# Kernel tuning notes

Hardware: AMD Instinct MI355X
Metric: run time of the kernel (lower is better)

Reference implementation:

```python
import jax, jax.numpy as jnp
import numpy as np

N_NODES = 100000
N_EDGES = 1600000
IN_DIM = 256
HID_DIM = 64
NUM_CLASSES = 32
NEG_SLOPE = 0.01  # F.leaky_relu default


def setup_inputs() -> dict:
    key = jax.random.key(0)
    k1, k2, k3, k4, k5, k6 = jax.random.split(key, 6)
    return {
        "local_features": jax.random.normal(k1, (N_NODES, IN_DIM), dtype=jnp.float32),
        "edge_index": jax.random.randint(k2, (2, N_EDGES), 0, N_NODES, dtype=jnp.int64),
        "weight1": jax.random.uniform(k3, (IN_DIM, HID_DIM), dtype=jnp.float32),
        "weight2": jax.random.uniform(k4, (HID_DIM, NUM_CLASSES), dtype=jnp.float32),
        "att_weight1": jax.random.uniform(k5, (2 * HID_DIM, 1), dtype=jnp.float32),
        "att_weight2": jax.random.uniform(k6, (2 * NUM_CLASSES, 1), dtype=jnp.float32),
    }


def _gat_attention_aggregate(H, a, src, dst, n_nodes):
    # H: [N, D], a: [2D, 1]. Edge score = leaky_relu([H_src||H_dst] @ a)
    # computed without materializing [E, 2D]: split a into src/dst halves.
    d = H.shape[1]
    s_score = (H @ a[:d]).squeeze(-1)   # [N]
    d_score = (H @ a[d:]).squeeze(-1)   # [N]
    e = jax.nn.leaky_relu(s_score[src] + d_score[dst], NEG_SLOPE)  # [E]
    # segment softmax over each row (grouped by src), as torch.sparse.softmax(dim=1)
    m = jax.ops.segment_max(e, src, num_segments=n_nodes)          # [N]
    ex = jnp.exp(e - m[src])                                       # [E]
    denom = jax.ops.segment_sum(ex, src, num_segments=n_nodes)     # [N]
    att = ex / denom[src]                                          # [E]
    # sparse mm: out[i] = sum_{(i,j) in E} att_ij * H[j]
    return jax.ops.segment_sum(att[:, None] * H[dst], src, num_segments=n_nodes)


def reference(local_features, edge_index, weight1, weight2, att_weight1, att_weight2):
    src, dst = edge_index[0], edge_index[1]
    n = local_features.shape[0]
    Hw1 = local_features @ weight1                                  # [N, HID]
    hidden = jax.nn.elu(_gat_attention_aggregate(Hw1, att_weight1, src, dst, n))
    Hw2 = hidden @ weight2                                          # [N, C]
    out = _gat_attention_aggregate(Hw2, att_weight2, src, dst, n)
    return jax.nn.log_softmax(out, axis=1)
```

## Files before the change

kernel.cpp:

```cpp
#include <hip/hip_runtime.h>
#include <math.h>

#define IN_DIM 256
#define HID 64
#define NC 32
#define NEG 0.01f
#define INF_NEG -1e30f
#define SX 36
#define SX2 68
#define MAXNBK 512
#define SLOT 8256
#define BCAP 12288
#define BIN_CHUNK 4096

static inline int ceil_div(int a, int b){ return (a + b - 1) / b; }

static __device__ __forceinline__ float lrelu(float x){ return x > 0.f ? x : NEG * x; }


__global__ __launch_bounds__(256) void bin_kernel(const int* __restrict__ src,
      const int* __restrict__ dst, int* __restrict__ cursor,
      unsigned int* __restrict__ tmp, int E, int nbk){
  __shared__ unsigned int payload[BIN_CHUNK];
  __shared__ unsigned short bid[BIN_CHUNK];
  __shared__ int cnt[MAXNBK];
  __shared__ int lofs[MAXNBK];
  __shared__ int gbase[MAXNBK];
  __shared__ int s2[256];
  int tid = threadIdx.x;
  int beg = blockIdx.x * BIN_CHUNK;
  int end = min(E, beg + BIN_CHUNK);
  int len = end - beg;

  for (int i = tid; i < MAXNBK; i += 256) cnt[i] = 0;
  __syncthreads();
  for (int e = beg + tid; e < end; e += 256)
    atomicAdd(&cnt[src[e] >> 8], 1);
  __syncthreads();
  int a0 = cnt[2 * tid], a1 = cnt[2 * tid + 1];
  int pair = a0 + a1;
  s2[tid] = pair; __syncthreads();
  int val = pair;
  for (int off = 1; off < 256; off <<= 1){
    int add = (tid >= off) ? s2[tid - off] : 0;
    __syncthreads();
    val += add; s2[tid] = val;
    __syncthreads();
  }
  int ep = val - pair;
  lofs[2 * tid] = ep;
  lofs[2 * tid + 1] = ep + a0;
  __syncthreads();
  for (int i = tid; i < nbk; i += 256){
    int c = cnt[i];
    gbase[i] = (c > 0) ? atomicAdd(&cursor[i], c) : 0;
  }
  __syncthreads();
  for (int i = tid; i < MAXNBK; i += 256) cnt[i] = 0;
  __syncthreads();
  for (int e = beg + tid; e < end; e += 256){
    int s = src[e];
    int b = s >> 8;
    int r = atomicAdd(&cnt[b], 1);
    int pos = lofs[b] + r;
    payload[pos] = ((unsigned)(s & 255) << 17) | (unsigned)dst[e];
    bid[pos] = (unsigned short)b;
  }
  __syncthreads();
  for (int pos = tid; pos < len; pos += 256){
    int b = bid[pos];
    int idx = pos - lofs[b];
    int g = gbase[b] + idx;
    if (g < SLOT) tmp[(size_t)b * SLOT + g] = payload[pos];
  }
}

__global__ __launch_bounds__(512) void bucket_base_kernel(const int* __restrict__ cursor,
      int* __restrict__ bbase, int nbk){
  __shared__ int sh[512];
  int tid = threadIdx.x;
  int v = (tid < nbk) ? min(cursor[tid], SLOT) : 0;
  sh[tid] = v; __syncthreads();
  int val = v;
  for (int off = 1; off < 512; off <<= 1){
    int add = (tid >= off) ? sh[tid - off] : 0;
    __syncthreads();
    val += add; sh[tid] = val;
    __syncthreads();
  }
  if (tid < nbk) bbase[tid] = val - v;
}

__global__ __launch_bounds__(256) void bucket_scatter_kernel(const unsigned int* __restrict__ tmp,
      const int* __restrict__ cursor, const int* __restrict__ bbase,
      int* __restrict__ row_ptr, int* __restrict__ csr, int n){
  __shared__ int cnt[256];
  __shared__ int cur[256];
  __shared__ int lbuf[BCAP];
  int tid = threadIdx.x;
  int b = blockIdx.x;
  int n0 = b << 8;
  int nn = min(256, n - n0);
  int len = min(cursor[b], SLOT);
  int segb = bbase[b];
  const unsigned int* T = tmp + (size_t)b * SLOT;
  cnt[tid] = 0;
  __syncthreads();
  for (int e = tid; e < len; e += 256) atomicAdd(&cnt[T[e] >> 17], 1);
  __syncthreads();
  int tv = cnt[tid];
  int val = tv;
  for (int off = 1; off < 256; off <<= 1){
    int add = (tid >= off) ? cnt[tid - off] : 0;
    __syncthreads();
    val += add; cnt[tid] = val;
    __syncthreads();
  }
  int excl = val - tv;
  cur[tid] = excl;
  if (tid < nn) row_ptr[n0 + tid] = segb + excl;
  if (n0 + nn == n && tid == 0) row_ptr[n] = segb + len;
  __syncthreads();
  if (len <= BCAP){
    for (int e = tid; e < len; e += 256){
      unsigned v = T[e];
      int pos = atomicAdd(&cur[v >> 17], 1);
      lbuf[pos] = (int)(v & 0x1FFFF);
    }
    __syncthreads();
    for (int e = tid; e < len; e += 256) csr[segb + e] = lbuf[e];
  } else {
    for (int e = tid; e < len; e += 256){
      unsigned v = T[e];
      int pos = atomicAdd(&cur[v >> 17], 1);
      csr[segb + pos] = (int)(v & 0x1FFFF);
    }
  }
}


__global__ void hist_kernel(const int* __restrict__ src, int* __restrict__ counts, int E){
  int i = blockIdx.x * blockDim.x + threadIdx.x;
  if (i < E) atomicAdd(&counts[src[i]], 1);
}
__global__ void scan_blocks_kernel(const int* __restrict__ counts, int* __restrict__ excl,
                                   int* __restrict__ bsums, int n){
  __shared__ int sh[256];
  int tid = threadIdx.x;
  int base = blockIdx.x * 1024 + tid * 4;
  int c[4]; int tsum = 0;
  #pragma unroll
  for (int j = 0; j < 4; j++){ int i = base + j; c[j] = (i < n) ? counts[i] : 0; tsum += c[j]; }
  sh[tid] = tsum; __syncthreads();
  int val = tsum;
  for (int off = 1; off < 256; off <<= 1){
    int add = (tid >= off) ? sh[tid - off] : 0;
    __syncthreads();
    val += add; sh[tid] = val;
    __syncthreads();
  }
  int p = val - tsum;
  #pragma unroll
  for (int j = 0; j < 4; j++){ int i = base + j; if (i < n) excl[i] = p; p += c[j]; }
  if (tid == 255) bsums[blockIdx.x] = val;
}
__global__ void scan_sums_kernel(int* __restrict__ bsums, int* __restrict__ row_ptr,
                                 int nb, int n, int E){
  __shared__ int sh[256];
  int tid = threadIdx.x;
  int v = (tid < nb) ? bsums[tid] : 0;
  sh[tid] = v; __syncthreads();
  int val = v;
  for (int off = 1; off < 256; off <<= 1){
    int add = (tid >= off) ? sh[tid - off] : 0;
    __syncthreads();
    val += add; sh[tid] = val;
    __syncthreads();
  }
  if (tid < nb) bsums[tid] = val - v;
  if (tid == 0) row_ptr[n] = E;
}
__global__ void add_offsets_kernel(int* __restrict__ excl, const int* __restrict__ bsums, int n){
  int i = blockIdx.x * 1024 + threadIdx.x;
  if (i < n) excl[i] += bsums[blockIdx.x];
}
__global__ void scatter_kernel(const int* __restrict__ src, const int* __restrict__ dst,
                               const int* __restrict__ row_ptr, int* __restrict__ fill,
                               int* __restrict__ csr, int E){
  int i = blockIdx.x * blockDim.x + threadIdx.x;
  if (i >= E) return;
  int s = src[i];
  int pos = row_ptr[s] + atomicAdd(&fill[s], 1);
  csr[pos] = dst[i];
}


__global__ __launch_bounds__(256) void gemm1_kernel(const float* __restrict__ X, const float* __restrict__ W,
      const float* __restrict__ a, float* __restrict__ H,
      float* __restrict__ svec, float* __restrict__ dvec, int n){
  __shared__ float xs[64 * SX];
  __shared__ float ws[32 * 64];
  int tid = threadIdx.x;
  int r0 = blockIdx.x * 64;
  int tr = tid >> 4;
  int tc = tid & 15;
  int srow = tid >> 3, sc8 = tid & 7;

  float4 pfx[2], pfw[2];
  #pragma unroll
  for (int p = 0; p < 2; p++){
    int row = p * 32 + srow;
    int gr = r0 + row;
    pfx[p] = make_float4(0.f, 0.f, 0.f, 0.f);
    if (gr < n) pfx[p] = *(const float4*)(X + (size_t)gr * IN_DIM + sc8 * 4);
  }
  #pragma unroll
  for (int p = 0; p < 2; p++){
    int idx = p * 256 + tid;
    int k = idx >> 4, c4 = idx & 15;
    pfw[p] = *(const float4*)(W + (size_t)k * 64 + c4 * 4);
  }

  float acc[4][4];
  #pragma unroll
  for (int i = 0; i < 4; i++)
    #pragma unroll
    for (int j = 0; j < 4; j++) acc[i][j] = 0.f;

  for (int kb = 0; kb < 8; kb++){
    __syncthreads();
    #pragma unroll
    for (int p = 0; p < 2; p++){
      int row = p * 32 + srow;
      *(float4*)(xs + row * SX + sc8 * 4) = pfx[p];
    }
    #pragma unroll
    for (int p = 0; p < 2; p++){
      int idx = p * 256 + tid;
      int k = idx >> 4, c4 = idx & 15;
      *(float4*)(ws + k * 64 + c4 * 4) = pfw[p];
    }
    if (kb < 7){
      #pragma unroll
      for (int p = 0; p < 2; p++){
        int row = p * 32 + srow;
        int gr = r0 + row;
        pfx[p] = make_float4(0.f, 0.f, 0.f, 0.f);
        if (gr < n) pfx[p] = *(const float4*)(X + (size_t)gr * IN_DIM + (kb + 1) * 32 + sc8 * 4);
      }
      #pragma unroll
      for (int p = 0; p < 2; p++){
        int idx = p * 256 + tid;
        int k = idx >> 4, c4 = idx & 15;
        pfw[p] = *(const float4*)(W + (size_t)((kb + 1) * 32 + k) * 64 + c4 * 4);
      }
    }
    __syncthreads();
    #pragma unroll
    for (int kq = 0; kq < 8; kq++){
      float xr[4][4];
      #pragma unroll
      for (int i = 0; i < 4; i++){
        float4 v = *(const float4*)(xs + (tr * 4 + i) * SX + kq * 4);
        xr[i][0] = v.x; xr[i][1] = v.y; xr[i][2] = v.z; xr[i][3] = v.w;
      }
      #pragma unroll
      for (int dk = 0; dk < 4; dk++){
        float4 w4 = *(const float4*)(ws + (size_t)(kq * 4 + dk) * 64 + tc * 4);
        float wv[4] = {w4.x, w4.y, w4.z, w4.w};
        #pragma unroll
        for (int i = 0; i < 4; i++)
          #pragma unroll
          for (int j = 0; j < 4; j++) acc[i][j] = fmaf(xr[i][dk], wv[j], acc[i][j]);
      }
    }
  }

  float av[4], bv[4];
  #pragma unroll
  for (int j = 0; j < 4; j++){ av[j] = a[tc * 4 + j]; bv[j] = a[64 + tc * 4 + j]; }
  float sp[4], dp[4];
  #pragma unroll
  for (int i = 0; i < 4; i++){
    float s = 0.f, d = 0.f;
    #pragma unroll
    for (int j = 0; j < 4; j++){ s = fmaf(acc[i][j], av[j], s); d = fmaf(acc[i][j], bv[j], d); }
    sp[i] = s; dp[i] = d;
  }
  #pragma unroll
  for (int off = 1; off < 16; off <<= 1){
    #pragma unroll
    for (int i = 0; i < 4; i++){
      sp[i] += __shfl_xor(sp[i], off, 16);
      dp[i] += __shfl_xor(dp[i], off, 16);
    }
  }
  #pragma unroll
  for (int i = 0; i < 4; i++){
    int r = r0 + tr * 4 + i;
    if (r < n){
      *(float4*)(H + (size_t)r * 64 + tc * 4) = make_float4(acc[i][0], acc[i][1], acc[i][2], acc[i][3]);
      if (tc == 0){ svec[r] = sp[i]; dvec[r] = dp[i]; }
    }
  }
}


__global__ __launch_bounds__(256) void gemm2_kernel(const float* __restrict__ X, const float* __restrict__ W,
      const float* __restrict__ a, float* __restrict__ H,
      float* __restrict__ svec, float* __restrict__ dvec, int n){
  __shared__ float xs[64 * SX2];
  __shared__ float ws[64 * 32];
  int tid = threadIdx.x;
  int r0 = blockIdx.x * 64;
  int tr = tid >> 4;
  int tc = tid & 15;

  #pragma unroll
  for (int p = 0; p < 4; p++){
    int lin = p * 256 + tid;
    int row = lin >> 4;
    int c4 = lin & 15;
    int gr = r0 + row;
    float4 v = make_float4(0.f, 0.f, 0.f, 0.f);
    if (gr < n) v = *(const float4*)(X + (size_t)gr * HID + c4 * 4);
    *(float4*)(xs + row * SX2 + c4 * 4) = v;
  }
  #pragma unroll
  for (int p = 0; p < 2; p++){
    int lin = p * 256 + tid;
    int k = lin >> 3, c4 = lin & 7;
    *(float4*)(ws + k * 32 + c4 * 4) = *(const float4*)(W + (size_t)k * 32 + c4 * 4);
  }
  __syncthreads();

  float acc[4][2];
  #pragma unroll
  for (int i = 0; i < 4; i++){ acc[i][0] = 0.f; acc[i][1] = 0.f; }

  #pragma unroll
  for (int kq = 0; kq < 16; kq++){
    float xr[4][4];
    #pragma unroll
    for (int i = 0; i < 4; i++){
      float4 v = *(const float4*)(xs + (tr * 4 + i) * SX2 + kq * 4);
      xr[i][0] = v.x; xr[i][1] = v.y; xr[i][2] = v.z; xr[i][3] = v.w;
    }
    #pragma unroll
    for (int dk = 0; dk < 4; dk++){
      float2 w2 = *(const float2*)(ws + (size_t)(kq * 4 + dk) * 32 + tc * 2);
      #pragma unroll
      for (int i = 0; i < 4; i++){
        acc[i][0] = fmaf(xr[i][dk], w2.x, acc[i][0]);
        acc[i][1] = fmaf(xr[i][dk], w2.y, acc[i][1]);
      }
    }
  }

  float a0 = a[tc * 2], a1 = a[tc * 2 + 1];
  float b0 = a[32 + tc * 2], b1 = a[32 + tc * 2 + 1];
  float sp[4], dp[4];
  #pragma unroll
  for (int i = 0; i < 4; i++){
    sp[i] = fmaf(acc[i][0], a0, acc[i][1] * a1);
    dp[i] = fmaf(acc[i][0], b0, acc[i][1] * b1);
  }
  #pragma unroll
  for (int off = 1; off < 16; off <<= 1){
    #pragma unroll
    for (int i = 0; i < 4; i++){
      sp[i] += __shfl_xor(sp[i], off, 16);
      dp[i] += __shfl_xor(dp[i], off, 16);
    }
  }
  #pragma unroll
  for (int i = 0; i < 4; i++){
    int r = r0 + tr * 4 + i;
    if (r < n){
      *(float2*)(H + (size_t)r * NC + tc * 2) = make_float2(acc[i][0], acc[i][1]);
      if (tc == 0){ svec[r] = sp[i]; dvec[r] = dp[i]; }
    }
  }
}


__global__ __launch_bounds__(256) void agg1_kernel(const float* __restrict__ H, const float* __restrict__ sv,
      const float* __restrict__ dv, const int* __restrict__ row_ptr, const int* __restrict__ csr,
      float* __restrict__ out, int n){
  int t = blockIdx.x * 256 + threadIdx.x;
  int g = t >> 4, fl = t & 15;
  if (g >= n) return;
  int beg = row_ptr[g], end = row_ptr[g + 1];
  float si = sv[g];
  float m = INF_NEG, l = 0.f;
  float ox = 0.f, oy = 0.f, oz = 0.f, ow = 0.f;

  for (int cb = beg; cb < end; cb += 32){
    int ce = min(cb + 32, end);
    int e0 = cb + fl, e1 = cb + 16 + fl;
    int d0 = 0, d1 = 0;
    float ev0 = INF_NEG, ev1 = INF_NEG;
    if (e0 < ce){ d0 = csr[e0]; ev0 = lrelu(si + dv[d0]); }
    if (e1 < ce){ d1 = csr[e1]; ev1 = lrelu(si + dv[d1]); }
    float lm = fmaxf(ev0, ev1);
    #pragma unroll
    for (int off = 1; off < 16; off <<= 1) lm = fmaxf(lm, __shfl_xor(lm, off, 16));
    float nm = fmaxf(m, lm);
    float alpha = __expf(m - nm);
    m = nm;
    ev0 = __expf(ev0 - nm);
    ev1 = __expf(ev1 - nm);
    float ll = ev0 + ev1;
    #pragma unroll
    for (int off = 1; off < 16; off <<= 1) ll += __shfl_xor(ll, off, 16);
    l = l * alpha + ll;
    ox *= alpha; oy *= alpha; oz *= alpha; ow *= alpha;
    #pragma unroll
    for (int jj = 0; jj < 16; jj++){
      float wgt = __shfl(ev0, jj, 16);
      int dd = __shfl(d0, jj, 16);
      float4 v = *(const float4*)(H + (size_t)dd * 64 + fl * 4);
      ox = fmaf(wgt, v.x, ox); oy = fmaf(wgt, v.y, oy);
      oz = fmaf(wgt, v.z, oz); ow = fmaf(wgt, v.w, ow);
    }
    if (ce - cb > 16){
      #pragma unroll
      for (int jj = 0; jj < 16; jj++){
        float wgt = __shfl(ev1, jj, 16);
        int dd = __shfl(d1, jj, 16);
        float4 v = *(const float4*)(H + (size_t)dd * 64 + fl * 4);
        ox = fmaf(wgt, v.x, ox); oy = fmaf(wgt, v.y, oy);
        oz = fmaf(wgt, v.z, oz); ow = fmaf(wgt, v.w, ow);
      }
    }
  }
  float inv = (l > 0.f) ? 1.f / l : 0.f;
  ox *= inv; oy *= inv; oz *= inv; ow *= inv;
  ox = ox > 0.f ? ox : __expf(ox) - 1.f;
  oy = oy > 0.f ? oy : __expf(oy) - 1.f;
  oz = oz > 0.f ? oz : __expf(oz) - 1.f;
  ow = ow > 0.f ? ow : __expf(ow) - 1.f;
  *(float4*)(out + (size_t)g * 64 + fl * 4) = make_float4(ox, oy, oz, ow);
}


__global__ __launch_bounds__(256) void agg2_kernel(const float* __restrict__ H, const float* __restrict__ sv,
      const float* __restrict__ dv, const int* __restrict__ row_ptr, const int* __restrict__ csr,
      float* __restrict__ out, int n){
  int t = blockIdx.x * 256 + threadIdx.x;
  int g = t >> 3, fl = t & 7;
  if (g >= n) return;
  int beg = row_ptr[g], end = row_ptr[g + 1];
  float si = sv[g];
  float m = INF_NEG, l = 0.f;
  float ox = 0.f, oy = 0.f, oz = 0.f, ow = 0.f;

  for (int cb = beg; cb < end; cb += 32){
    int ce = min(cb + 32, end);
    float ev[4]; int dd4[4];
    float lm = INF_NEG;
    #pragma unroll
    for (int s = 0; s < 4; s++){
      int e = cb + s * 8 + fl;
      ev[s] = INF_NEG; dd4[s] = 0;
      if (e < ce){ dd4[s] = csr[e]; ev[s] = lrelu(si + dv[dd4[s]]); }
      lm = fmaxf(lm, ev[s]);
    }
    #pragma unroll
    for (int off = 1; off < 8; off <<= 1) lm = fmaxf(lm, __shfl_xor(lm, off, 8));
    float nm = fmaxf(m, lm);
    float alpha = __expf(m - nm);
    m = nm;
    float ll = 0.f;
    #pragma unroll
    for (int s = 0; s < 4; s++){ ev[s] = __expf(ev[s] - nm); ll += ev[s]; }
    #pragma unroll
    for (int off = 1; off < 8; off <<= 1) ll += __shfl_xor(ll, off, 8);
    l = l * alpha + ll;
    ox *= alpha; oy *= alpha; oz *= alpha; ow *= alpha;
    #pragma unroll
    for (int s = 0; s < 4; s++){
      if (ce - cb > s * 8){
        #pragma unroll
        for (int jj = 0; jj < 8; jj++){
          float wgt = __shfl(ev[s], jj, 8);
          int dd = __shfl(dd4[s], jj, 8);
          float4 v = *(const float4*)(H + (size_t)dd * 32 + fl * 4);
          ox = fmaf(wgt, v.x, ox); oy = fmaf(wgt, v.y, oy);
          oz = fmaf(wgt, v.z, oz); ow = fmaf(wgt, v.w, ow);
        }
      }
    }
  }
  float inv = (l > 0.f) ? 1.f / l : 0.f;
  ox *= inv; oy *= inv; oz *= inv; ow *= inv;
  float tm = fmaxf(fmaxf(ox, oy), fmaxf(oz, ow));
  #pragma unroll
  for (int off = 1; off < 8; off <<= 1) tm = fmaxf(tm, __shfl_xor(tm, off, 8));
  float se = __expf(ox - tm) + __expf(oy - tm) + __expf(oz - tm) + __expf(ow - tm);
  #pragma unroll
  for (int off = 1; off < 8; off <<= 1) se += __shfl_xor(se, off, 8);
  float lg = tm + __logf(se);
  *(float4*)(out + (size_t)g * 32 + fl * 4) = make_float4(ox - lg, oy - lg, oz - lg, ow - lg);
}


extern "C" void kernel_launch(void* const* d_in, const int* in_sizes, int n_in,
                              void* d_out, int out_size, void* d_ws, size_t ws_size,
                              hipStream_t stream) {
  (void)n_in; (void)out_size; (void)ws_size;
  const float* X  = (const float*)d_in[0];
  const int*   EI = (const int*)d_in[1];
  const float* W1 = (const float*)d_in[2];
  const float* W2 = (const float*)d_in[3];
  const float* A1 = (const float*)d_in[4];
  const float* A2 = (const float*)d_in[5];
  float* out = (float*)d_out;

  int N = in_sizes[0] / IN_DIM;
  int E = in_sizes[1] / 2;
  const int* src = EI;
  const int* dst = EI + E;

  auto align_up = [](size_t x){ return (x + 511) & ~(size_t)511; };
  char* w = (char*)d_ws;
  int* counts  = (int*)w;   w += align_up((size_t)N * 4);
  int* cursor  = (int*)w;   w += align_up((size_t)MAXNBK * 4);
  int* bbase   = (int*)w;   w += align_up((size_t)MAXNBK * 4);
  int* row_ptr = (int*)w;   w += align_up((size_t)(N + 1) * 4);
  int* bsums   = (int*)w;   w += align_up(1024);
  int* csr     = (int*)w;   w += align_up((size_t)E * 4);
  float* H1    = (float*)w; w += align_up((size_t)N * 64 * 4);
  float* hid   = (float*)w; w += align_up((size_t)N * 64 * 4);
  float* s1    = (float*)w; w += align_up((size_t)N * 4);
  float* d1    = (float*)w; w += align_up((size_t)N * 4);
  float* s2    = (float*)w; w += align_up((size_t)N * 4);
  float* d2    = (float*)w; w += align_up((size_t)N * 4);
  float* H2    = H1;
  unsigned int* tmp = (unsigned int*)hid;

  int nbk = ceil_div(N, 256);

  if (N <= (1 << 17) && nbk <= MAXNBK && (size_t)nbk * SLOT <= (size_t)N * 64){
    hipMemsetAsync(cursor, 0, (size_t)nbk * 4, stream);
    bin_kernel<<<ceil_div(E, BIN_CHUNK), 256, 0, stream>>>(src, dst, cursor, tmp, E, nbk);
    bucket_base_kernel<<<1, 512, 0, stream>>>(cursor, bbase, nbk);
    bucket_scatter_kernel<<<nbk, 256, 0, stream>>>(tmp, cursor, bbase, row_ptr, csr, N);
  } else {
    int nb = ceil_div(N, 1024);
    hipMemsetAsync(counts, 0, (size_t)N * 4, stream);
    hist_kernel<<<ceil_div(E, 256), 256, 0, stream>>>(src, counts, E);
    scan_blocks_kernel<<<nb, 256, 0, stream>>>(counts, row_ptr, bsums, N);
    scan_sums_kernel<<<1, 256, 0, stream>>>(bsums, row_ptr, nb, N, E);
    add_offsets_kernel<<<nb, 1024, 0, stream>>>(row_ptr, bsums, N);
    hipMemsetAsync(counts, 0, (size_t)N * 4, stream);
    scatter_kernel<<<ceil_div(E, 256), 256, 0, stream>>>(src, dst, row_ptr, counts, csr, E);
  }

  gemm1_kernel<<<ceil_div(N, 64), 256, 0, stream>>>(X, W1, A1, H1, s1, d1, N);
  agg1_kernel<<<ceil_div(N * 16, 256), 256, 0, stream>>>(H1, s1, d1, row_ptr, csr, hid, N);
  gemm2_kernel<<<ceil_div(N, 64), 256, 0, stream>>>(hid, W2, A2, H2, s2, d2, N);
  agg2_kernel<<<ceil_div(N * 8, 256), 256, 0, stream>>>(H2, s2, d2, row_ptr, csr, out, N);
}
```

Measured before the change: 354.4 us.

## Split gemm1 K-dimension across two half-blocks with 4x8 register tiles

Reorganizes the first-layer GEMM so each thread computes a 4x8 output tile over half of each 32-wide K chunk. The two halves of the block then reduce their partial sums through shared memory before the attention-score epilogue. This raises the FMA-to-LDS-load ratio per thread, which should ease shared-memory bandwidth pressure. The cost is more registers per thread, an extra shared-memory reduction with two barriers, and an epilogue in which only half the threads do the work.

New measurement: 351.3 us. Within noise of the previous version (-0.9%).

```diff
diff --git a/kernel.cpp b/kernel.cpp
--- a/kernel.cpp
+++ b/kernel.cpp
@@ -202,8 +202,11 @@
   __shared__ float ws[32 * 64];
   int tid = threadIdx.x;
   int r0 = blockIdx.x * 64;
-  int tr = tid >> 4;
-  int tc = tid & 15;
+  int h  = tid >> 7;
+  int lt = tid & 127;
+  int rg = lt >> 3;
+  int cg = lt & 7;
+  int koff = h * 16;
   int srow = tid >> 3, sc8 = tid & 7;
 
   float4 pfx[2], pfw[2];
@@ -221,11 +224,11 @@
     pfw[p] = *(const float4*)(W + (size_t)k * 64 + c4 * 4);
   }
 
-  float acc[4][4];
+  float acc[4][8];
   #pragma unroll
   for (int i = 0; i < 4; i++)
     #pragma unroll
-    for (int j = 0; j < 4; j++) acc[i][j] = 0.f;
+    for (int j = 0; j < 8; j++) acc[i][j] = 0.f;
 
   for (int kb = 0; kb < 8; kb++){
     __syncthreads();
@@ -257,50 +260,85 @@
     }
     __syncthreads();
     #pragma unroll
-    for (int kq = 0; kq < 8; kq++){
+    for (int kq0 = 0; kq0 < 4; kq0++){
+      int kbase = koff + kq0 * 4;
       float xr[4][4];
       #pragma unroll
       for (int i = 0; i < 4; i++){
-        float4 v = *(const float4*)(xs + (tr * 4 + i) * SX + kq * 4);
+        float4 v = *(const float4*)(xs + (rg * 4 + i) * SX + kbase);
         xr[i][0] = v.x; xr[i][1] = v.y; xr[i][2] = v.z; xr[i][3] = v.w;
       }
       #pragma unroll
       for (int dk = 0; dk < 4; dk++){
-        float4 w4 = *(const float4*)(ws + (size_t)(kq * 4 + dk) * 64 + tc * 4);
-        float wv[4] = {w4.x, w4.y, w4.z, w4.w};
+        float4 wA = *(const float4*)(ws + (size_t)(kbase + dk) * 64 + cg * 8);
+        float4 wB = *(const float4*)(ws + (size_t)(kbase + dk) * 64 + cg * 8 + 4);
         #pragma unroll
-        for (int i = 0; i < 4; i++)
-          #pragma unroll
-          for (int j = 0; j < 4; j++) acc[i][j] = fmaf(xr[i][dk], wv[j], acc[i][j]);
-      }
-    }
-  }
-
-  float av[4], bv[4];
-  #pragma unroll
-  for (int j = 0; j < 4; j++){ av[j] = a[tc * 4 + j]; bv[j] = a[64 + tc * 4 + j]; }
-  float sp[4], dp[4];
-  #pragma unroll
-  for (int i = 0; i < 4; i++){
-    float s = 0.f, d = 0.f;
-    #pragma unroll
-    for (int j = 0; j < 4; j++){ s = fmaf(acc[i][j], av[j], s); d = fmaf(acc[i][j], bv[j], d); }
-    sp[i] = s; dp[i] = d;
-  }
-  #pragma unroll
-  for (int off = 1; off < 16; off <<= 1){
+        for (int i = 0; i < 4; i++){
+          acc[i][0] = fmaf(xr[i][dk], wA.x, acc[i][0]);
+          acc[i][1] = fmaf(xr[i][dk], wA.y, acc[i][1]);
+          acc[i][2] = fmaf(xr[i][dk], wA.z, acc[i][2]);
+          acc[i][3] = fmaf(xr[i][dk], wA.w, acc[i][3]);
+          acc[i][4] = fmaf(xr[i][dk], wB.x, acc[i][4]);
+          acc[i][5] = fmaf(xr[i][dk], wB.y, acc[i][5]);
+          acc[i][6] = fmaf(xr[i][dk], wB.z, acc[i][6]);
+          acc[i][7] = fmaf(xr[i][dk], wB.w, acc[i][7]);
+        }
+      }
+    }
+  }
+
+  __syncthreads();
+  if (h == 1){
     #pragma unroll
     for (int i = 0; i < 4; i++){
-      sp[i] += __shfl_xor(sp[i], off, 16);
-      dp[i] += __shfl_xor(dp[i], off, 16);
-    }
-  }
-  #pragma unroll
-  for (int i = 0; i < 4; i++){
-    int r = r0 + tr * 4 + i;
-    if (r < n){
-      *(float4*)(H + (size_t)r * 64 + tc * 4) = make_float4(acc[i][0], acc[i][1], acc[i][2], acc[i][3]);
-      if (tc == 0){ svec[r] = sp[i]; dvec[r] = dp[i]; }
+      #pragma unroll
+      for (int jj = 0; jj < 2; jj++)
+        *(float4*)(xs + (i * 2 + jj) * 512 + lt * 4) =
+            make_float4(acc[i][jj * 4], acc[i][jj * 4 + 1], acc[i][jj * 4 + 2], acc[i][jj * 4 + 3]);
+    }
+  }
+  __syncthreads();
+  if (h == 0){
+    #pragma unroll
+    for (int i = 0; i < 4; i++){
+      #pragma unroll
+      for (int jj = 0; jj < 2; jj++){
+        float4 v = *(const float4*)(xs + (i * 2 + jj) * 512 + lt * 4);
+        acc[i][jj * 4]     += v.x;
+        acc[i][jj * 4 + 1] += v.y;
+        acc[i][jj * 4 + 2] += v.z;
+        acc[i][jj * 4 + 3] += v.w;
+      }
+    }
+    float av[8], bv[8];
+    #pragma unroll
+    for (int j = 0; j < 8; j++){ av[j] = a[cg * 8 + j]; bv[j] = a[64 + cg * 8 + j]; }
+    float sp[4], dp[4];
+    #pragma unroll
+    for (int i = 0; i < 4; i++){
+      float s = 0.f, d = 0.f;
+      #pragma unroll
+      for (int j = 0; j < 8; j++){ s = fmaf(acc[i][j], av[j], s); d = fmaf(acc[i][j], bv[j], d); }
+      sp[i] = s; dp[i] = d;
+    }
+    #pragma unroll
+    for (int off = 1; off < 8; off <<= 1){
+      #pragma unroll
+      for (int i = 0; i < 4; i++){
+        sp[i] += __shfl_xor(sp[i], off, 8);
+        dp[i] += __shfl_xor(dp[i], off, 8);
+      }
+    }
+    #pragma unroll
+    for (int i = 0; i < 4; i++){
+      int r = r0 + rg * 4 + i;
+      if (r < n){
+        *(float4*)(H + (size_t)r * 64 + cg * 8) =
+            make_float4(acc[i][0], acc[i][1], acc[i][2], acc[i][3]);
+        *(float4*)(H + (size_t)r * 64 + cg * 8 + 4) =
+            make_float4(acc[i][4], acc[i][5], acc[i][6], acc[i][7]);
+        if (cg == 0){ svec[r] = sp[i]; dvec[r] = dp[i]; }
+      }
     }
   }
 }
```
